# Kernel optimization log

Measured on AMD Instinct MI355X. Metric: run time of the kernel, lower is better.

Reference implementation:

```python
import jax, jax.numpy as jnp
import numpy as np

ALPHA = 1.0
BETA = 0.5

B, N, E = 4096, 4096, 16384


def setup_inputs() -> dict:
    key = jax.random.key(0)
    k1, k2, k3, k4, k5 = jax.random.split(key, 5)
    outputs = jax.random.normal(k1, (B, N), dtype=jnp.float32)
    targets = jax.random.uniform(k2, (B, N), dtype=jnp.float32)
    # per-node level weight (equivalent to node_levels dict -> level_weights lookup)
    level_w = jax.random.uniform(k3, (N,), dtype=jnp.float32)
    edge_src = jax.random.randint(k4, (E,), 0, N, dtype=jnp.int32)  # parent i
    edge_dst = jax.random.randint(k5, (E,), 0, N, dtype=jnp.int32)  # child  j
    return {"outputs": outputs, "targets": targets, "level_w": level_w,
            "edge_src": edge_src, "edge_dst": edge_dst}


def reference(outputs, targets, level_w, edge_src, edge_dst):
    # BCEWithLogits, reduction='none': softplus(x) - x*t (numerically stable)
    bce = jax.nn.softplus(outputs) - outputs * targets          # [B, N]
    weighted_bce = bce * level_w[None, :]                        # [B, N]

    probs = jax.nn.sigmoid(outputs)                              # [B, N]
    # for each edge (i=parent, j=child): consistency[:, j] += relu(p[:, j] - p[:, i])
    diff = jax.nn.relu(probs[:, edge_dst] - probs[:, edge_src])  # [B, E]
    consistency = jnp.zeros_like(probs).at[:, edge_dst].add(diff)  # [B, N]

    return ALPHA * weighted_bce.mean() + BETA * consistency.mean()
```

## Files before the change

### kernel.cpp

```cpp
#include <hip/hip_runtime.h>
#include <math.h>


#define ALPHA_C 1.0f
#define BETA_C  0.5f

constexpr int B = 4096;
constexpr int N = 4096;
constexpr int E = 16384;
constexpr int THREADS = 512;
constexpr int R = 4;

typedef _Float16 h4 __attribute__((ext_vector_type(4)));

__global__ __launch_bounds__(64) void init_out_kernel(float* out) {
    if (threadIdx.x == 0) out[0] = 0.0f;
}

__device__ __forceinline__ void fast_sig_sp(float x, float& p, float& sp) {
    float q = __expf(-fabsf(x));
    float d = 1.0f + q;
    float r = __builtin_amdgcn_rcpf(d);
    p  = (x >= 0.0f) ? r : q * r;
    sp = fmaxf(x, 0.0f) + __logf(d);
}

__global__ __launch_bounds__(THREADS, 8) void hier_loss_kernel(
    const float* __restrict__ outputs,
    const float* __restrict__ targets,
    const float* __restrict__ level_w,
    const int*   __restrict__ edge_src,
    const int*   __restrict__ edge_dst,
    float*       __restrict__ out)
{
    __shared__ h4 P[N];

    const int r0  = blockIdx.x * R;
    const int tid = threadIdx.x;

    const float4* out4 = (const float4*)outputs;
    const float4* tgt4 = (const float4*)targets;
    const float4* lw4  = (const float4*)level_w;

    float s1 = 0.0f;
#pragma unroll
    for (int j = 0; j < N / 4 / THREADS; ++j) {
        const int n4 = tid + j * THREADS;
        const float4 w = lw4[n4];
        const float wv[4] = {w.x, w.y, w.z, w.w};
        float4 xs[R], ts[R];
#pragma unroll
        for (int r = 0; r < R; ++r) {
            xs[r] = out4[(size_t)(r0 + r) * (N / 4) + n4];
            ts[r] = tgt4[(size_t)(r0 + r) * (N / 4) + n4];
        }
        h4 tmp[4];
#pragma unroll
        for (int r = 0; r < R; ++r) {
            const float xv[4] = {xs[r].x, xs[r].y, xs[r].z, xs[r].w};
            const float tv[4] = {ts[r].x, ts[r].y, ts[r].z, ts[r].w};
#pragma unroll
            for (int k = 0; k < 4; ++k) {
                float p, sp;
                fast_sig_sp(xv[k], p, sp);
                s1 = fmaf(wv[k], sp - xv[k] * tv[k], s1);
                tmp[k][r] = (_Float16)p;
            }
        }
#pragma unroll
        for (int k = 0; k < 4; ++k) P[4 * n4 + k] = tmp[k];
    }
    __syncthreads();

    h4 acc0 = {0, 0, 0, 0};
    h4 acc1 = {0, 0, 0, 0};
    const h4 zero = {0, 0, 0, 0};
    const int4* es4 = (const int4*)edge_src;
    const int4* ed4 = (const int4*)edge_dst;
#pragma unroll
    for (int j = 0; j < E / 4 / THREADS; ++j) {
        const int i = tid + j * THREADS;
        const int4 s = es4[i];
        const int4 d = ed4[i];
        h4 a0 = P[s.x], c0 = P[d.x];
        h4 a1 = P[s.y], c1 = P[d.y];
        h4 a2 = P[s.z], c2 = P[d.z];
        h4 a3 = P[s.w], c3 = P[d.w];
        acc0 += __builtin_elementwise_max(c0 - a0, zero);
        acc1 += __builtin_elementwise_max(c1 - a1, zero);
        acc0 += __builtin_elementwise_max(c2 - a2, zero);
        acc1 += __builtin_elementwise_max(c3 - a3, zero);
    }
    float s2 = 0.0f;
#pragma unroll
    for (int l = 0; l < 4; ++l) s2 += (float)acc0[l] + (float)acc1[l];

#pragma unroll
    for (int off = 32; off > 0; off >>= 1) {
        s1 += __shfl_down(s1, off, 64);
        s2 += __shfl_down(s2, off, 64);
    }
    __syncthreads();
    float* red = (float*)P;
    const int wave = tid >> 6;
    const int lane = tid & 63;
    if (lane == 0) { red[wave] = s1; red[8 + wave] = s2; }
    __syncthreads();
    if (tid == 0) {
        float a = 0.0f, c = 0.0f;
#pragma unroll
        for (int w = 0; w < 8; ++w) { a += red[w]; c += red[8 + w]; }
        const float inv = 1.0f / ((float)B * (float)N);
        atomicAdd(out, (ALPHA_C * a + BETA_C * c) * inv);
    }
}

extern "C" void kernel_launch(void* const* d_in, const int* in_sizes, int n_in,
                              void* d_out, int out_size, void* d_ws, size_t ws_size,
                              hipStream_t stream) {
    const float* outputs = (const float*)d_in[0];
    const float* targets = (const float*)d_in[1];
    const float* level_w = (const float*)d_in[2];
    const int*   edge_src = (const int*)d_in[3];
    const int*   edge_dst = (const int*)d_in[4];
    float* out = (float*)d_out;

    init_out_kernel<<<1, 64, 0, stream>>>(out);
    hier_loss_kernel<<<B / R, THREADS, 0, stream>>>(outputs, targets, level_w,
                                                    edge_src, edge_dst, out);
}
```

Before: 156.6 us.

## Process multiple row groups per block with double-buffered LDS and register-cached edges

Each 1024-thread block now handles four groups of four rows. Edge indices are loaded into registers once and reused across all groups, and the next group's inputs are prefetched while the current group is gathered. Two probability buffers in LDS allow a single barrier per group. This cuts the repeated edge-index traffic and overlaps global loads with the LDS gather. The cost is fewer blocks (one per CU), a doubled LDS footprint and more register pressure, which lowers occupancy and latency hiding.

```diff
diff --git a/kernel.cpp b/kernel.cpp
--- a/kernel.cpp
+++ b/kernel.cpp
@@ -8,8 +8,11 @@
 constexpr int B = 4096;
 constexpr int N = 4096;
 constexpr int E = 16384;
-constexpr int THREADS = 512;
+constexpr int THREADS = 1024;
 constexpr int R = 4;
+constexpr int G = 4;
+constexpr int GRID = B / (R * G);
+constexpr int EJ = E / 4 / THREADS;
 
 typedef _Float16 h4 __attribute__((ext_vector_type(4)));
 
@@ -25,7 +28,7 @@
     sp = fmaxf(x, 0.0f) + __logf(d);
 }
 
-__global__ __launch_bounds__(THREADS, 8) void hier_loss_kernel(
+__global__ __launch_bounds__(THREADS, 4) void hier_loss_kernel(
     const float* __restrict__ outputs,
     const float* __restrict__ targets,
     const float* __restrict__ level_w,
@@ -33,32 +36,45 @@
     const int*   __restrict__ edge_dst,
     float*       __restrict__ out)
 {
-    __shared__ h4 P[N];
+    __shared__ h4 Pbuf[2][N];
 
-    const int r0  = blockIdx.x * R;
-    const int tid = threadIdx.x;
+    const int tid  = threadIdx.x;
+    const int row0 = blockIdx.x * (R * G);
 
     const float4* out4 = (const float4*)outputs;
     const float4* tgt4 = (const float4*)targets;
     const float4* lw4  = (const float4*)level_w;
+    const int4*   es4  = (const int4*)edge_src;
+    const int4*   ed4  = (const int4*)edge_dst;
 
-    float s1 = 0.0f;
+    int4 sc[EJ], dc[EJ];
 #pragma unroll
-    for (int j = 0; j < N / 4 / THREADS; ++j) {
-        const int n4 = tid + j * THREADS;
-        const float4 w = lw4[n4];
-        const float wv[4] = {w.x, w.y, w.z, w.w};
-        float4 xs[R], ts[R];
+    for (int j = 0; j < EJ; ++j) {
+        sc[j] = es4[tid + j * THREADS];
+        dc[j] = ed4[tid + j * THREADS];
+    }
+    const float4 w = lw4[tid];
+    const float wv[4] = {w.x, w.y, w.z, w.w};
+
+    float4 xs[R], tt[R];
 #pragma unroll
-        for (int r = 0; r < R; ++r) {
-            xs[r] = out4[(size_t)(r0 + r) * (N / 4) + n4];
-            ts[r] = tgt4[(size_t)(r0 + r) * (N / 4) + n4];
-        }
+    for (int r = 0; r < R; ++r) {
+        const size_t off = (size_t)(row0 + r) * (N / 4) + tid;
+        xs[r] = out4[off];
+        tt[r] = tgt4[off];
+    }
+
+    float s1 = 0.0f, s2 = 0.0f;
+
+#pragma unroll
+    for (int g = 0; g < G; ++g) {
+        h4* P = Pbuf[g & 1];
+
         h4 tmp[4];
 #pragma unroll
         for (int r = 0; r < R; ++r) {
             const float xv[4] = {xs[r].x, xs[r].y, xs[r].z, xs[r].w};
-            const float tv[4] = {ts[r].x, ts[r].y, ts[r].z, ts[r].w};
+            const float tv[4] = {tt[r].x, tt[r].y, tt[r].z, tt[r].w};
 #pragma unroll
             for (int k = 0; k < 4; ++k) {
                 float p, sp;
@@ -68,32 +84,36 @@
             }
         }
 #pragma unroll
-        for (int k = 0; k < 4; ++k) P[4 * n4 + k] = tmp[k];
+        for (int k = 0; k < 4; ++k) P[4 * tid + k] = tmp[k];
+
+        if (g + 1 < G) {
+#pragma unroll
+            for (int r = 0; r < R; ++r) {
+                const size_t off = (size_t)(row0 + (g + 1) * R + r) * (N / 4) + tid;
+                xs[r] = out4[off];
+                tt[r] = tgt4[off];
+            }
+        }
+
+        asm volatile("s_waitcnt lgkmcnt(0)\n\ts_barrier" ::: "memory");
+
+        h4 acc0 = {0, 0, 0, 0};
+        h4 acc1 = {0, 0, 0, 0};
+        const h4 zero = {0, 0, 0, 0};
+#pragma unroll
+        for (int j = 0; j < EJ; ++j) {
+            h4 a0 = P[sc[j].x], c0 = P[dc[j].x];
+            h4 a1 = P[sc[j].y], c1 = P[dc[j].y];
+            h4 a2 = P[sc[j].z], c2 = P[dc[j].z];
+            h4 a3 = P[sc[j].w], c3 = P[dc[j].w];
+            acc0 += __builtin_elementwise_max(c0 - a0, zero);
+            acc1 += __builtin_elementwise_max(c1 - a1, zero);
+            acc0 += __builtin_elementwise_max(c2 - a2, zero);
+            acc1 += __builtin_elementwise_max(c3 - a3, zero);
+        }
+#pragma unroll
+        for (int l = 0; l < 4; ++l) s2 += (float)acc0[l] + (float)acc1[l];
     }
-    __syncthreads();
-
-    h4 acc0 = {0, 0, 0, 0};
-    h4 acc1 = {0, 0, 0, 0};
-    const h4 zero = {0, 0, 0, 0};
-    const int4* es4 = (const int4*)edge_src;
-    const int4* ed4 = (const int4*)edge_dst;
-#pragma unroll
-    for (int j = 0; j < E / 4 / THREADS; ++j) {
-        const int i = tid + j * THREADS;
-        const int4 s = es4[i];
-        const int4 d = ed4[i];
-        h4 a0 = P[s.x], c0 = P[d.x];
-        h4 a1 = P[s.y], c1 = P[d.y];
-        h4 a2 = P[s.z], c2 = P[d.z];
-        h4 a3 = P[s.w], c3 = P[d.w];
-        acc0 += __builtin_elementwise_max(c0 - a0, zero);
-        acc1 += __builtin_elementwise_max(c1 - a1, zero);
-        acc0 += __builtin_elementwise_max(c2 - a2, zero);
-        acc1 += __builtin_elementwise_max(c3 - a3, zero);
-    }
-    float s2 = 0.0f;
-#pragma unroll
-    for (int l = 0; l < 4; ++l) s2 += (float)acc0[l] + (float)acc1[l];
 
 #pragma unroll
     for (int off = 32; off > 0; off >>= 1) {
@@ -101,15 +121,15 @@
         s2 += __shfl_down(s2, off, 64);
     }
     __syncthreads();
-    float* red = (float*)P;
+    float* red = (float*)&Pbuf[0][0];
     const int wave = tid >> 6;
     const int lane = tid & 63;
-    if (lane == 0) { red[wave] = s1; red[8 + wave] = s2; }
+    if (lane == 0) { red[wave] = s1; red[16 + wave] = s2; }
     __syncthreads();
     if (tid == 0) {
         float a = 0.0f, c = 0.0f;
 #pragma unroll
-        for (int w = 0; w < 8; ++w) { a += red[w]; c += red[8 + w]; }
+        for (int wv2 = 0; wv2 < 16; ++wv2) { a += red[wv2]; c += red[16 + wv2]; }
         const float inv = 1.0f / ((float)B * (float)N);
         atomicAdd(out, (ALPHA_C * a + BETA_C * c) * inv);
     }
@@ -126,6 +146,6 @@
     float* out = (float*)d_out;
 
     init_out_kernel<<<1, 64, 0, stream>>>(out);
-    hier_loss_kernel<<<B / R, THREADS, 0, stream>>>(outputs, targets, level_w,
-                                                    edge_src, edge_dst, out);
+    hier_loss_kernel<<<GRID, THREADS, 0, stream>>>(outputs, targets, level_w,
+                                                   edge_src, edge_dst, out);
 }
```

New measurement: 172.5 us. +10.1%, slower.

## Split fused loss into BCE/sigmoid kernel and edge-gather kernel via fp16 workspace

Applied to the files above, without the earlier changes.

Splits the single fused kernel into two. The first computes the weighted BCE sum and writes fp16 sigmoid probabilities, packed 8 rows per node, to a global workspace. The second reloads each 8-row group into LDS and gathers over the edges with 8-wide half vectors. This halves the number of edge-index loads per row and gives each phase its own occupancy profile, at the cost of an extra global write and read of the probabilities plus a second launch.

```diff
diff --git a/kernel.cpp b/kernel.cpp
--- a/kernel.cpp
+++ b/kernel.cpp
@@ -8,10 +8,8 @@
 constexpr int B = 4096;
 constexpr int N = 4096;
 constexpr int E = 16384;
-constexpr int THREADS = 512;
-constexpr int R = 4;
 
-typedef _Float16 h4 __attribute__((ext_vector_type(4)));
+typedef _Float16 h8 __attribute__((ext_vector_type(8)));
 
 __global__ __launch_bounds__(64) void init_out_kernel(float* out) {
     if (threadIdx.x == 0) out[0] = 0.0f;
@@ -25,93 +23,119 @@
     sp = fmaxf(x, 0.0f) + __logf(d);
 }
 
-__global__ __launch_bounds__(THREADS, 8) void hier_loss_kernel(
+constexpr int T1 = 1024;
+__global__ __launch_bounds__(T1, 4)
+__attribute__((amdgpu_waves_per_eu(4, 4)))
+void k1_bce_sig(
     const float* __restrict__ outputs,
     const float* __restrict__ targets,
     const float* __restrict__ level_w,
-    const int*   __restrict__ edge_src,
-    const int*   __restrict__ edge_dst,
+    _Float16*    __restrict__ Pint,
     float*       __restrict__ out)
 {
-    __shared__ h4 P[N];
-
-    const int r0  = blockIdx.x * R;
+    __shared__ float red[16];
+    const int g   = blockIdx.x;
     const int tid = threadIdx.x;
 
     const float4* out4 = (const float4*)outputs;
     const float4* tgt4 = (const float4*)targets;
-    const float4* lw4  = (const float4*)level_w;
+
+    float4 xs[8], ts[8];
+#pragma unroll
+    for (int r = 0; r < 8; ++r) {
+        const size_t off = (size_t)(8 * g + r) * (N / 4) + tid;
+        xs[r] = out4[off];
+        ts[r] = tgt4[off];
+    }
+    const float4 w = ((const float4*)level_w)[tid];
+    const float wv[4] = {w.x, w.y, w.z, w.w};
 
     float s1 = 0.0f;
+    h8 pv[4];
 #pragma unroll
-    for (int j = 0; j < N / 4 / THREADS; ++j) {
-        const int n4 = tid + j * THREADS;
-        const float4 w = lw4[n4];
-        const float wv[4] = {w.x, w.y, w.z, w.w};
-        float4 xs[R], ts[R];
+    for (int r = 0; r < 8; ++r) {
+        const float xv[4] = {xs[r].x, xs[r].y, xs[r].z, xs[r].w};
+        const float tv[4] = {ts[r].x, ts[r].y, ts[r].z, ts[r].w};
 #pragma unroll
-        for (int r = 0; r < R; ++r) {
-            xs[r] = out4[(size_t)(r0 + r) * (N / 4) + n4];
-            ts[r] = tgt4[(size_t)(r0 + r) * (N / 4) + n4];
+        for (int k = 0; k < 4; ++k) {
+            float p, sp;
+            fast_sig_sp(xv[k], p, sp);
+            s1 = fmaf(wv[k], sp - xv[k] * tv[k], s1);
+            pv[k][r] = (_Float16)p;
         }
-        h4 tmp[4];
+    }
+    h8* PG = (h8*)(Pint + (size_t)g * (N * 8));
 #pragma unroll
-        for (int r = 0; r < R; ++r) {
-            const float xv[4] = {xs[r].x, xs[r].y, xs[r].z, xs[r].w};
-            const float tv[4] = {ts[r].x, ts[r].y, ts[r].z, ts[r].w};
+    for (int k = 0; k < 4; ++k) PG[4 * tid + k] = pv[k];
+
 #pragma unroll
-            for (int k = 0; k < 4; ++k) {
-                float p, sp;
-                fast_sig_sp(xv[k], p, sp);
-                s1 = fmaf(wv[k], sp - xv[k] * tv[k], s1);
-                tmp[k][r] = (_Float16)p;
-            }
-        }
+    for (int off = 32; off > 0; off >>= 1) s1 += __shfl_down(s1, off, 64);
+    const int wave = tid >> 6, lane = tid & 63;
+    if (lane == 0) red[wave] = s1;
+    __syncthreads();
+    if (tid == 0) {
+        float a = 0.0f;
 #pragma unroll
-        for (int k = 0; k < 4; ++k) P[4 * n4 + k] = tmp[k];
+        for (int i = 0; i < 16; ++i) a += red[i];
+        atomicAdd(out, ALPHA_C * a / ((float)B * (float)N));
     }
+}
+
+constexpr int T2 = 1024;
+__global__ __launch_bounds__(T2, 4) void k2_edges(
+    const _Float16* __restrict__ Pint,
+    const int*      __restrict__ edge_src,
+    const int*      __restrict__ edge_dst,
+    float*          __restrict__ out)
+{
+    __shared__ h8 Pl[N];
+    __shared__ float red[16];
+
+    const int g   = blockIdx.x;
+    const int tid = threadIdx.x;
+
+    const int4* es4 = (const int4*)edge_src;
+    const int4* ed4 = (const int4*)edge_dst;
+    int4 sc[4], dc[4];
+#pragma unroll
+    for (int j = 0; j < 4; ++j) {
+        sc[j] = es4[tid + j * T2];
+        dc[j] = ed4[tid + j * T2];
+    }
+
+    const h8* PG = (const h8*)(Pint + (size_t)g * (N * 8));
+#pragma unroll
+    for (int j = 0; j < N / T2; ++j)
+        Pl[tid + j * T2] = PG[tid + j * T2];
     __syncthreads();
 
-    h4 acc0 = {0, 0, 0, 0};
-    h4 acc1 = {0, 0, 0, 0};
-    const h4 zero = {0, 0, 0, 0};
-    const int4* es4 = (const int4*)edge_src;
-    const int4* ed4 = (const int4*)edge_dst;
+    float s2 = 0.0f;
+    const h8 zero = {0, 0, 0, 0, 0, 0, 0, 0};
 #pragma unroll
-    for (int j = 0; j < E / 4 / THREADS; ++j) {
-        const int i = tid + j * THREADS;
-        const int4 s = es4[i];
-        const int4 d = ed4[i];
-        h4 a0 = P[s.x], c0 = P[d.x];
-        h4 a1 = P[s.y], c1 = P[d.y];
-        h4 a2 = P[s.z], c2 = P[d.z];
-        h4 a3 = P[s.w], c3 = P[d.w];
-        acc0 += __builtin_elementwise_max(c0 - a0, zero);
-        acc1 += __builtin_elementwise_max(c1 - a1, zero);
-        acc0 += __builtin_elementwise_max(c2 - a2, zero);
-        acc1 += __builtin_elementwise_max(c3 - a3, zero);
+    for (int j = 0; j < 4; ++j) {
+        h8 acc = zero;
+        h8 a0 = Pl[sc[j].x], c0 = Pl[dc[j].x];
+        h8 a1 = Pl[sc[j].y], c1 = Pl[dc[j].y];
+        h8 a2 = Pl[sc[j].z], c2 = Pl[dc[j].z];
+        h8 a3 = Pl[sc[j].w], c3 = Pl[dc[j].w];
+        acc += __builtin_elementwise_max(c0 - a0, zero);
+        acc += __builtin_elementwise_max(c1 - a1, zero);
+        acc += __builtin_elementwise_max(c2 - a2, zero);
+        acc += __builtin_elementwise_max(c3 - a3, zero);
+#pragma unroll
+        for (int l = 0; l < 8; ++l) s2 += (float)acc[l];
     }
-    float s2 = 0.0f;
-#pragma unroll
-    for (int l = 0; l < 4; ++l) s2 += (float)acc0[l] + (float)acc1[l];
 
 #pragma unroll
-    for (int off = 32; off > 0; off >>= 1) {
-        s1 += __shfl_down(s1, off, 64);
-        s2 += __shfl_down(s2, off, 64);
-    }
-    __syncthreads();
-    float* red = (float*)P;
-    const int wave = tid >> 6;
-    const int lane = tid & 63;
-    if (lane == 0) { red[wave] = s1; red[8 + wave] = s2; }
+    for (int off = 32; off > 0; off >>= 1) s2 += __shfl_down(s2, off, 64);
+    const int wave = tid >> 6, lane = tid & 63;
+    if (lane == 0) red[wave] = s2;
     __syncthreads();
     if (tid == 0) {
-        float a = 0.0f, c = 0.0f;
+        float c = 0.0f;
 #pragma unroll
-        for (int w = 0; w < 8; ++w) { a += red[w]; c += red[8 + w]; }
-        const float inv = 1.0f / ((float)B * (float)N);
-        atomicAdd(out, (ALPHA_C * a + BETA_C * c) * inv);
+        for (int i = 0; i < 16; ++i) c += red[i];
+        atomicAdd(out, BETA_C * c / ((float)B * (float)N));
     }
 }
 
@@ -124,8 +148,9 @@
     const int*   edge_src = (const int*)d_in[3];
     const int*   edge_dst = (const int*)d_in[4];
     float* out = (float*)d_out;
+    _Float16* Pint = (_Float16*)d_ws;
 
     init_out_kernel<<<1, 64, 0, stream>>>(out);
-    hier_loss_kernel<<<B / R, THREADS, 0, stream>>>(outputs, targets, level_w,
-                                                    edge_src, edge_dst, out);
+    k1_bce_sig<<<B / 8, T1, 0, stream>>>(outputs, targets, level_w, Pint, out);
+    k2_edges<<<B / 8, T2, 0, stream>>>(Pint, edge_src, edge_dst, out);
 }
```

Result: slower. 177.8 us (+13.5%).
